# Performance work log

Measured on AMD Instinct MI355X. Metric: run time of the kernel, lower is better.

## Reference

```python
import jax, jax.numpy as jnp
import numpy as np

NVOC = 32000
DIM = 512
HID = 512
NLAYERS = 2
SEQ = 128
BATCH = 32


def setup_inputs() -> dict:
    key = jax.random.key(0)
    ks = jax.random.split(key, 8)
    tokens = jax.random.randint(ks[0], (SEQ, BATCH), 0, NVOC, dtype=jnp.int32)
    emb = jax.random.uniform(ks[1], (NVOC, DIM), minval=-0.1, maxval=0.1, dtype=jnp.float32)
    # xavier-uniform-ish init for gate matrices
    def xav(k, shape):
        fan_in, fan_out = shape[1], shape[0]
        lim = jnp.sqrt(6.0 / (fan_in + fan_out))
        return jax.random.uniform(k, shape, minval=-lim, maxval=lim, dtype=jnp.float32)
    W0 = xav(ks[2], (4 * HID, DIM))     # layer 0 input weights
    W1 = xav(ks[3], (4 * HID, HID))     # layer 1 input weights
    U0 = xav(ks[4], (4 * HID, HID))
    U1 = xav(ks[5], (4 * HID, HID))
    b = jnp.zeros((4 * HID,), jnp.float32)
    dec_w = jax.random.uniform(ks[6], (NVOC, HID), minval=-0.1, maxval=0.1, dtype=jnp.float32)
    dec_b = jnp.zeros((NVOC,), jnp.float32)
    return {"tokens": tokens, "emb": emb, "W0": W0, "W1": W1,
            "U0": U0, "U1": U1, "b": b, "dec_w": dec_w, "dec_b": dec_b}


def _lstm_forward(tokens, emb, W0, W1, U0, U1, b, dec_w, dec_b):
    # dropout in eval mode (identity)
    x = emb[tokens]  # [S, B, DIM]
    Ws = [W0, W1]
    Us = [U0, U1]
    h0 = jnp.zeros((NLAYERS, BATCH, HID), x.dtype)
    c0 = jnp.zeros((NLAYERS, BATCH, HID), x.dtype)

    def step(carry, x_t):
        h_tot, c_tot = carry
        new_h, new_c = [], []
        inp = x_t
        for l in range(NLAYERS):
            gates = inp @ Ws[l].T + h_tot[l] @ Us[l].T + b  # [B, 4H]
            i_g, f_g, g_g, o_g = jnp.split(gates, 4, axis=1)
            i_g = jax.nn.sigmoid(i_g)
            f_g = jax.nn.sigmoid(f_g)
            o_g = jax.nn.sigmoid(o_g)
            g_g = jnp.tanh(g_g)
            c_new = f_g * c_tot[l] + i_g * g_g
            h_new = o_g * jnp.tanh(c_new)
            new_h.append(h_new)
            new_c.append(c_new)
            inp = h_new
        return (jnp.stack(new_h), jnp.stack(new_c)), new_h[-1]

    (_, _), outs = jax.lax.scan(step, (h0, c0), x)  # outs: [S, B, HID]
    decoded = outs @ dec_w.T + dec_b  # [S, B, NVOC]
    return decoded


def reference(tokens, emb, W0, W1, U0, U1, b, dec_w, dec_b):
    return _lstm_forward(tokens, emb, W0, W1, U0, U1, b, dec_w, dec_b)
```

## Files before the change

### kernel.cpp

```cpp
#include <hip/hip_runtime.h>
#include <hip/hip_bf16.h>


#define NVOC 32000
#define DIM  512
#define HID  512
#define SEQ  128
#define BAT  32
#define NB   64
#define NDEC 192
#define NTILE (32 * 250)

typedef short s8v __attribute__((ext_vector_type(8)));
typedef short s4v __attribute__((ext_vector_type(4)));
typedef float f4v __attribute__((ext_vector_type(4)));
typedef unsigned long long u64;

__device__ __forceinline__ short f2bf(float f) {
    unsigned u = __builtin_bit_cast(unsigned, f);
    unsigned r = (u + 0x7fffu + ((u >> 16) & 1u)) >> 16;
    return (short)r;
}
__device__ __forceinline__ float bf2f(short s) {
    unsigned u = ((unsigned)(unsigned short)s) << 16;
    return __builtin_bit_cast(float, u);
}
__device__ __forceinline__ float sigm(float x) { return 1.f / (1.f + __expf(-x)); }
__device__ __forceinline__ float ftanh(float x) {
    float e = __expf(2.f * x);
    return 1.f - 2.f / (e + 1.f);
}

__device__ __forceinline__ f4v mf16(s8v a, s8v b, f4v c) {
    return __builtin_amdgcn_mfma_f32_16x16x32_bf16(a, b, c, 0, 0, 0);
}

__device__ __forceinline__ u64 cohload8(const short* p) {
    return __hip_atomic_load((const u64*)p, __ATOMIC_RELAXED,
                             __HIP_MEMORY_SCOPE_AGENT);
}
__device__ __forceinline__ void cohstore2(short* p, unsigned short v) {
    __hip_atomic_store((unsigned short*)p, v, __ATOMIC_RELAXED,
                       __HIP_MEMORY_SCOPE_AGENT);
}

__device__ __forceinline__ void pollwait(const unsigned* bar, int l,
                                         unsigned tA, unsigned tB) {
    const unsigned* fp = bar + l;
    const unsigned tgt = (l < 32) ? tA : tB;
    while (true) {
        unsigned v = __hip_atomic_load(fp, __ATOMIC_RELAXED,
                                       __HIP_MEMORY_SCOPE_AGENT);
        if (__all((int)(v >= tgt))) break;
    }
}
__device__ __forceinline__ void poll32s(const unsigned* f, int l, unsigned tgt) {
    const unsigned* p = f + (l & 31);
    while (true) {
        unsigned v = __hip_atomic_load(p, __ATOMIC_RELAXED,
                                       __HIP_MEMORY_SCOPE_AGENT);
        if (__all((int)(v >= tgt))) break;
        __builtin_amdgcn_s_sleep(16);
    }
}

__global__ __launch_bounds__(256) void prep_dec(const float* __restrict__ dw,
                                                short* __restrict__ dbf)
{
    int id = blockIdx.x * 256 + threadIdx.x;
    if (id >= (NVOC * DIM) / 4) return;
    int e = id * 4;
    float4 v = *(const float4*)(dw + e);
    s4v o; o[0] = f2bf(v.x); o[1] = f2bf(v.y); o[2] = f2bf(v.z); o[3] = f2bf(v.w);
    *(s4v*)(dbf + e) = o;
}

__global__ __launch_bounds__(256) void prep_w0(const float* __restrict__ W0,
                                               short* __restrict__ w0h,
                                               short* __restrict__ w0l)
{
    int id = blockIdx.x * 256 + threadIdx.x;
    if (id >= 2048 * 512) return;
    float v = W0[id];
    short h = f2bf(v);
    w0h[id] = h;
    w0l[id] = f2bf(v - bf2f(h));
}

__global__ __launch_bounds__(256) void embed_k(const int* __restrict__ toks,
                                               const float* __restrict__ emb,
                                               short* __restrict__ xemb)
{
    int id = blockIdx.x * 256 + threadIdx.x;
    if (id >= (SEQ * BAT * DIM) / 4) return;
    int e  = id * 4;
    int tb = e >> 9;
    int k4 = e & 511;
    int tok = toks[tb];
    float4 v = *(const float4*)(emb + (size_t)tok * DIM + k4);
    s4v o; o[0] = f2bf(v.x); o[1] = f2bf(v.y); o[2] = f2bf(v.z); o[3] = f2bf(v.w);
    *(s4v*)(xemb + e) = o;
}

__global__ __launch_bounds__(256) void init_k(short* __restrict__ hbuf,
                                              unsigned* __restrict__ bar)
{
    int id = blockIdx.x * 256 + threadIdx.x;
    if (id < 10 * BAT * HID) hbuf[id] = 0;
    if (id < 64) bar[id] = 0;
}

__global__ __launch_bounds__(256) void gx_gemm(
    const short* __restrict__ A,
    const short* __restrict__ Bh,
    const short* __restrict__ Bl,
    float* __restrict__ out)
{
    const int nb = blockIdx.x & 15, mb = blockIdx.x >> 4;
    const int m0 = mb * 128, n0 = nb * 128;
    __shared__ short Alds[128][40];
    __shared__ short Bhl[128][40];
    __shared__ short Bll[128][40];
    const int tid = threadIdx.x, l = tid & 63, w = tid >> 6;
    const int wr = w >> 1, wc = w & 1;
    const int lr = l & 15, kg = l >> 4;

    f4v acc[4][4];
    #pragma unroll
    for (int mi = 0; mi < 4; ++mi)
        #pragma unroll
        for (int ni = 0; ni < 4; ++ni) {
            acc[mi][ni][0] = 0.f; acc[mi][ni][1] = 0.f;
            acc[mi][ni][2] = 0.f; acc[mi][ni][3] = 0.f;
        }

    for (int kt = 0; kt < 16; ++kt) {
        #pragma unroll
        for (int i = 0; i < 2; ++i) {
            int c = tid + i * 256;
            int row = c >> 2, q = (c & 3) << 3;
            *(s8v*)&Alds[row][q] = *(const s8v*)(A  + (size_t)(m0 + row) * 512 + kt * 32 + q);
            *(s8v*)&Bhl[row][q]  = *(const s8v*)(Bh + (size_t)(n0 + row) * 512 + kt * 32 + q);
            *(s8v*)&Bll[row][q]  = *(const s8v*)(Bl + (size_t)(n0 + row) * 512 + kt * 32 + q);
        }
        __syncthreads();
        s8v af[4], bhf[4], blf[4];
        #pragma unroll
        for (int i = 0; i < 4; ++i) {
            af[i]  = *(const s8v*)&Alds[wr * 64 + i * 16 + lr][kg * 8];
            bhf[i] = *(const s8v*)&Bhl[wc * 64 + i * 16 + lr][kg * 8];
            blf[i] = *(const s8v*)&Bll[wc * 64 + i * 16 + lr][kg * 8];
        }
        #pragma unroll
        for (int mi = 0; mi < 4; ++mi)
            #pragma unroll
            for (int ni = 0; ni < 4; ++ni) {
                acc[mi][ni] = mf16(af[mi], bhf[ni], acc[mi][ni]);
                acc[mi][ni] = mf16(af[mi], blf[ni], acc[mi][ni]);
            }
        __syncthreads();
    }

    #pragma unroll
    for (int mi = 0; mi < 4; ++mi)
        #pragma unroll
        for (int ni = 0; ni < 4; ++ni) {
            int n = n0 + wc * 64 + ni * 16 + lr;
            #pragma unroll
            for (int r = 0; r < 4; ++r) {
                int m = m0 + wr * 64 + mi * 16 + kg * 4 + r;
                out[(size_t)m * 2048 + n] = acc[mi][ni][r];
            }
        }
}

__global__ __launch_bounds__(512, 1) void rnn_k(
    const float* __restrict__ W1f, const float* __restrict__ U0f,
    const float* __restrict__ U1f,
    const float* __restrict__ bias,
    const float* __restrict__ Gx,
    short* __restrict__ hbuf,
    short* __restrict__ adec,
    const short* __restrict__ dbf,
    const float* __restrict__ db,
    float* __restrict__ out,
    unsigned* __restrict__ bar)
{
    const int tid = threadIdx.x;
    const int bx  = blockIdx.x;
    const int w2  = tid >> 6;
    const int l   = tid & 63;
    const int lr  = l & 15;
    const int kg  = l >> 4;

    __shared__ short Alds[32][520];
    __shared__ float gbuf[2][4][16][33];
    __shared__ float pbuf[2][4][16][33];
    __shared__ s8v AdT[4][132];
    __shared__ s8v BdT[4][132];

    if (bx >= NB) {
        const int d  = bx - NB;
        const int wm = w2 >> 2;
        const int wn = w2 & 3;
        const int drow = tid >> 2, dq = tid & 3;
        int lastmb = -1;
        for (int tile = d; tile < NTILE; tile += NDEC) {
            const int mb = tile / 250, nbt = tile - mb * 250;
            const int m0 = mb * 128, n0 = nbt * 128;
            if (mb != lastmb) {
                if (w2 == 0) poll32s(bar + 32, l, (unsigned)(4 * mb + 5));
                __syncthreads();
                lastmb = mb;
            }
            f4v acc[4][2];
            #pragma unroll
            for (int mi = 0; mi < 4; ++mi)
                #pragma unroll
                for (int ni = 0; ni < 2; ++ni) {
                    acc[mi][ni][0] = 0.f; acc[mi][ni][1] = 0.f;
                    acc[mi][ni][2] = 0.f; acc[mi][ni][3] = 0.f;
                }
            for (int kt = 0; kt < 16; ++kt) {
                AdT[dq][drow] = *(const s8v*)(adec + (size_t)(m0 + drow) * 512 + kt * 32 + dq * 8);
                BdT[dq][drow] = *(const s8v*)(dbf  + (size_t)(n0 + drow) * 512 + kt * 32 + dq * 8);
                __syncthreads();
                s8v af[4], bfr[2];
                #pragma unroll
                for (int i = 0; i < 4; ++i)
                    af[i] = AdT[kg][wm * 64 + i * 16 + lr];
                #pragma unroll
                for (int j = 0; j < 2; ++j)
                    bfr[j] = BdT[kg][wn * 32 + j * 16 + lr];
                #pragma unroll
                for (int mi = 0; mi < 4; ++mi)
                    #pragma unroll
                    for (int ni = 0; ni < 2; ++ni)
                        acc[mi][ni] = mf16(af[mi], bfr[ni], acc[mi][ni]);
                __syncthreads();
            }
            #pragma unroll
            for (int mi = 0; mi < 4; ++mi)
                #pragma unroll
                for (int ni = 0; ni < 2; ++ni) {
                    int n = n0 + wn * 32 + ni * 16 + lr;
                    float bb = db[n];
                    #pragma unroll
                    for (int r = 0; r < 4; ++r) {
                        int m = m0 + wm * 64 + mi * 16 + kg * 4 + r;
                        out[(size_t)m * NVOC + n] = acc[mi][ni][r] + bb;
                    }
                }
        }
        return;
    }

    const int bl    = bx;
    const int layer = bl >> 5;
    const int j0    = (bl & 31) * 16;
    const int g     = w2 & 3;
    const int kh    = w2 >> 2;

    const int eb = tid >> 4;
    const int ej = tid & 15;
    const int jj = j0 + ej;
    const float bi = bias[jj];
    const float bf_ = bias[512 + jj];
    const float bg = bias[1024 + jj];
    const float bo = bias[1536 + jj];
    float cst = 0.f;

    short* h0r = hbuf;
    short* h1r = hbuf + 8 * BAT * HID;

    auto stageK512 = [&](const short* s) {
        u64 va[8];
        #pragma unroll
        for (int i = 0; i < 8; ++i) {
            int c = tid + i * 512;
            va[i] = cohload8(s + (c >> 7) * HID + (c & 127) * 4);
        }
        #pragma unroll
        for (int i = 0; i < 8; ++i) {
            int c = tid + i * 512;
            *(u64*)&Alds[c >> 7][(c & 127) * 4] = va[i];
        }
    };
    auto mfma8 = [&](const s8v* WH, const s8v* WL, float (&dst)[2][4][16][33]) {
        f4v a0h = {0.f, 0.f, 0.f, 0.f};
        f4v a0l = a0h, a1h = a0h, a1l = a0h;
        #pragma unroll
        for (int ks = 0; ks < 8; ++ks) {
            const int k = kh * 256 + ks * 32 + kg * 8;
            s8v a0 = *(const s8v*)&Alds[lr][k];
            s8v a1 = *(const s8v*)&Alds[16 + lr][k];
            a0h = mf16(a0, WH[ks], a0h);
            a0l = mf16(a0, WL[ks], a0l);
            a1h = mf16(a1, WH[ks], a1h);
            a1l = mf16(a1, WL[ks], a1l);
        }
        #pragma unroll
        for (int r = 0; r < 4; ++r) {
            dst[kh][g][lr][kg * 4 + r]      = a0h[r] + a0l[r];
            dst[kh][g][lr][16 + kg * 4 + r] = a1h[r] + a1l[r];
        }
    };
    const int gr = g * 512 + j0 + lr;
    auto loadw = [&](const float* M, s8v* WH, s8v* WL) {
        #pragma unroll
        for (int ks = 0; ks < 8; ++ks) {
            const float* src = M + (size_t)gr * 512 + kh * 256 + ks * 32 + kg * 8;
            float4 va = *(const float4*)src;
            float4 vb = *(const float4*)(src + 4);
            float vv[8] = {va.x, va.y, va.z, va.w, vb.x, vb.y, vb.z, vb.w};
            s8v hi, lo;
            #pragma unroll
            for (int e = 0; e < 8; ++e) {
                short h = f2bf(vv[e]);
                hi[e] = h; lo[e] = f2bf(vv[e] - bf2f(h));
            }
            WH[ks] = hi; WL[ks] = lo;
        }
    };

    if (layer == 0) {
        s8v wh[8], wl[8];
        loadw(U0f, wh, wl);
        for (int it = 0; it < SEQ; ++it) {
            const unsigned itu = (unsigned)it;
            const float* gp = Gx + ((size_t)it * BAT + eb) * 2048 + jj;
            float gx0 = gp[0], gx1 = gp[512], gx2 = gp[1024], gx3 = gp[1536];
            if (it > 0) {
                if (w2 == 0) pollwait(bar, l, itu, (it >= 7) ? itu - 6u : 0u);
                __syncthreads();
            }
            stageK512(h0r + ((it + 7) & 7) * (BAT * HID));
            __syncthreads();
            mfma8(wh, wl, gbuf);
            __syncthreads();
            float si = gbuf[0][0][ej][eb] + gbuf[1][0][ej][eb] + gx0;
            float sf = gbuf[0][1][ej][eb] + gbuf[1][1][ej][eb] + gx1;
            float sg = gbuf[0][2][ej][eb] + gbuf[1][2][ej][eb] + gx2;
            float so = gbuf[0][3][ej][eb] + gbuf[1][3][ej][eb] + gx3;
            float gi = sigm(si + bi);
            float gf = sigm(sf + bf_);
            float gg = ftanh(sg + bg);
            float go = sigm(so + bo);
            cst = gf * cst + gi * gg;
            unsigned short hs = (unsigned short)f2bf(go * ftanh(cst));
            cohstore2(h0r + (it & 7) * (BAT * HID) + eb * HID + jj, hs);
            asm volatile("s_waitcnt vmcnt(0)" ::: "memory");
            __syncthreads();
            if (tid == 0)
                __hip_atomic_store(bar + (bl & 31), itu + 1u,
                                   __ATOMIC_RELAXED, __HIP_MEMORY_SCOPE_AGENT);
        }
    } else {
        s8v whU[8], wlU[8], whW[8], wlW[8];
        loadw(U1f, whU, wlU);
        loadw(W1f, whW, wlW);
        if (w2 == 0) pollwait(bar, l, 1u, 0u);
        __syncthreads();
        stageK512(h0r);
        __syncthreads();
        mfma8(whW, wlW, pbuf);
        for (int it = 1; it <= SEQ; ++it) {
            const unsigned itu = (unsigned)it;
            if (w2 == 0) pollwait(bar, l, 0u, (it >= 2) ? itu : 0u);
            __syncthreads();
            stageK512(h1r + (it & 1) * (BAT * HID));
            __syncthreads();
            mfma8(whU, wlU, gbuf);
            __syncthreads();
            float si = gbuf[0][0][ej][eb] + gbuf[1][0][ej][eb]
                     + pbuf[0][0][ej][eb] + pbuf[1][0][ej][eb];
            float sf = gbuf[0][1][ej][eb] + gbuf[1][1][ej][eb]
                     + pbuf[0][1][ej][eb] + pbuf[1][1][ej][eb];
            float sg = gbuf[0][2][ej][eb] + gbuf[1][2][ej][eb]
                     + pbuf[0][2][ej][eb] + pbuf[1][2][ej][eb];
            float so = gbuf[0][3][ej][eb] + gbuf[1][3][ej][eb]
                     + pbuf[0][3][ej][eb] + pbuf[1][3][ej][eb];
            float gi = sigm(si + bi);
            float gf = sigm(sf + bf_);
            float gg = ftanh(sg + bg);
            float go = sigm(so + bo);
            cst = gf * cst + gi * gg;
            unsigned short hs = (unsigned short)f2bf(go * ftanh(cst));
            cohstore2(h1r + ((it + 1) & 1) * (BAT * HID) + eb * HID + jj, hs);
            cohstore2(adec + ((size_t)(it - 1) * BAT + eb) * HID + jj, hs);
            asm volatile("s_waitcnt vmcnt(0)" ::: "memory");
            __syncthreads();
            if (tid == 0)
                __hip_atomic_store(bar + 32 + (bl & 31), itu + 1u,
                                   __ATOMIC_RELAXED, __HIP_MEMORY_SCOPE_AGENT);
            if (it < SEQ) {
                if (w2 == 0) pollwait(bar, l, itu + 1u, 0u);
                __syncthreads();
                stageK512(h0r + (it & 7) * (BAT * HID));
                __syncthreads();
                mfma8(whW, wlW, pbuf);
            }
        }
    }
}

extern "C" void kernel_launch(void* const* d_in, const int* in_sizes, int n_in,
                              void* d_out, int out_size, void* d_ws, size_t ws_size,
                              hipStream_t stream)
{
    const int*   toks = (const int*)d_in[0];
    const float* emb  = (const float*)d_in[1];
    const float* W0   = (const float*)d_in[2];
    const float* W1   = (const float*)d_in[3];
    const float* U0   = (const float*)d_in[4];
    const float* U1   = (const float*)d_in[5];
    const float* bias = (const float*)d_in[6];
    const float* dw   = (const float*)d_in[7];
    const float* db   = (const float*)d_in[8];
    float* out = (float*)d_out;

    char* ws = (char*)d_ws;
    size_t off = 0;
    auto alloc = [&](size_t bytes) -> void* {
        void* p = ws + off;
        off += (bytes + 255) & ~(size_t)255;
        return p;
    };
    short*    dbf  = (short*)alloc((size_t)NVOC * DIM * 2);
    short*    xemb = (short*)alloc((size_t)SEQ * BAT * DIM * 2);
    short*    w0h  = (short*)alloc(2048ull * 512 * 2);
    short*    w0l  = (short*)alloc(2048ull * 512 * 2);
    float*    Gx   = (float*)alloc((size_t)SEQ * BAT * 2048 * 4);
    short*    hbuf = (short*)alloc(10ull * BAT * HID * 2);
    short*    adec = (short*)alloc((size_t)SEQ * BAT * HID * 2);
    unsigned* bar  = (unsigned*)alloc(256);

    prep_dec<<<(NVOC * DIM / 4 + 255) / 256, 256, 0, stream>>>(dw, dbf);
    prep_w0 <<<(2048 * 512 + 255) / 256, 256, 0, stream>>>(W0, w0h, w0l);
    embed_k <<<(SEQ * BAT * DIM / 4 + 255) / 256, 256, 0, stream>>>(toks, emb, xemb);
    init_k  <<<(10 * BAT * HID + 255) / 256, 256, 0, stream>>>(hbuf, bar);

    gx_gemm<<<32 * 16, 256, 0, stream>>>(xemb, w0h, w0l, Gx);

    rnn_k<<<NB + NDEC, 512, 0, stream>>>(W1, U0, U1, bias, Gx, hbuf, adec,
                                         dbf, db, out, bar);
}
```

Measured before the change: 793.4 us.

## Replace RNN flag barriers with sentinel-filled full-history h ring buffers

Each of the two recurrent layers now writes every timestep's hidden state into its own slot of a 129-slot buffer. Each buffer is pre-filled with an all-ones sentinel except slot 0. Consumers spin on the loaded 8-byte words until no 16-bit lane holds the sentinel, instead of polling per-block counters and doing a block barrier, waitcnt and flag store every step. This removes the per-step flag round-trip from the recurrence critical path. The layer-1 counter used by the decoder blocks is now only updated every 4 steps. In exchange, init writes a much larger buffer, and correctness relies on 0xFFFF never appearing as a real bf16 h value and on ordering of relaxed stores.

After: 699.0 us. 11.9% less time.

```diff
diff --git a/kernel.cpp b/kernel.cpp
--- a/kernel.cpp
+++ b/kernel.cpp
@@ -10,6 +10,7 @@
 #define NB   64
 #define NDEC 192
 #define NTILE (32 * 250)
+#define SLOT (BAT * HID)
 
 typedef short s8v __attribute__((ext_vector_type(8)));
 typedef short s4v __attribute__((ext_vector_type(4)));
@@ -44,16 +45,11 @@
                        __HIP_MEMORY_SCOPE_AGENT);
 }
 
-__device__ __forceinline__ void pollwait(const unsigned* bar, int l,
-                                         unsigned tA, unsigned tB) {
-    const unsigned* fp = bar + l;
-    const unsigned tgt = (l < 32) ? tA : tB;
-    while (true) {
-        unsigned v = __hip_atomic_load(fp, __ATOMIC_RELAXED,
-                                       __HIP_MEMORY_SCOPE_AGENT);
-        if (__all((int)(v >= tgt))) break;
-    }
-}
+__device__ __forceinline__ bool hasSent(u64 v) {
+    u64 n = ~v;
+    return ((n - 0x0001000100010001ull) & ~n & 0x8000800080008000ull) != 0ull;
+}
+
 __device__ __forceinline__ void poll32s(const unsigned* f, int l, unsigned tgt) {
     const unsigned* p = f + (l & 31);
     while (true) {
@@ -106,7 +102,12 @@
                                               unsigned* __restrict__ bar)
 {
     int id = blockIdx.x * 256 + threadIdx.x;
-    if (id < 10 * BAT * HID) hbuf[id] = 0;
+    const int ringU64 = 129 * SLOT / 4;
+    if (id < 2 * ringU64) {
+        int r = id % ringU64;
+        u64 v = (r < SLOT / 4) ? 0ull : 0xFFFFFFFFFFFFFFFFull;
+        ((u64*)hbuf)[id] = v;
+    }
     if (id < 64) bar[id] = 0;
 }
 
@@ -270,10 +271,10 @@
     const float bo = bias[1536 + jj];
     float cst = 0.f;
 
-    short* h0r = hbuf;
-    short* h1r = hbuf + 8 * BAT * HID;
-
-    auto stageK512 = [&](const short* s) {
+    short* ring0 = hbuf;
+    short* ring1 = hbuf + 129 * SLOT;
+
+    auto stageS = [&](const short* s) {
         u64 va[8];
         #pragma unroll
         for (int i = 0; i < 8; ++i) {
@@ -283,6 +284,8 @@
         #pragma unroll
         for (int i = 0; i < 8; ++i) {
             int c = tid + i * 512;
+            while (hasSent(va[i]))
+                va[i] = cohload8(s + (c >> 7) * HID + (c & 127) * 4);
             *(u64*)&Alds[c >> 7][(c & 127) * 4] = va[i];
         }
     };
@@ -327,14 +330,9 @@
         s8v wh[8], wl[8];
         loadw(U0f, wh, wl);
         for (int it = 0; it < SEQ; ++it) {
-            const unsigned itu = (unsigned)it;
             const float* gp = Gx + ((size_t)it * BAT + eb) * 2048 + jj;
             float gx0 = gp[0], gx1 = gp[512], gx2 = gp[1024], gx3 = gp[1536];
-            if (it > 0) {
-                if (w2 == 0) pollwait(bar, l, itu, (it >= 7) ? itu - 6u : 0u);
-                __syncthreads();
-            }
-            stageK512(h0r + ((it + 7) & 7) * (BAT * HID));
+            stageS(ring0 + (size_t)it * SLOT);
             __syncthreads();
             mfma8(wh, wl, gbuf);
             __syncthreads();
@@ -348,27 +346,17 @@
             float go = sigm(so + bo);
             cst = gf * cst + gi * gg;
             unsigned short hs = (unsigned short)f2bf(go * ftanh(cst));
-            cohstore2(h0r + (it & 7) * (BAT * HID) + eb * HID + jj, hs);
-            asm volatile("s_waitcnt vmcnt(0)" ::: "memory");
-            __syncthreads();
-            if (tid == 0)
-                __hip_atomic_store(bar + (bl & 31), itu + 1u,
-                                   __ATOMIC_RELAXED, __HIP_MEMORY_SCOPE_AGENT);
+            cohstore2(ring0 + (size_t)(it + 1) * SLOT + eb * HID + jj, hs);
         }
     } else {
         s8v whU[8], wlU[8], whW[8], wlW[8];
         loadw(U1f, whU, wlU);
         loadw(W1f, whW, wlW);
-        if (w2 == 0) pollwait(bar, l, 1u, 0u);
-        __syncthreads();
-        stageK512(h0r);
+        stageS(ring0 + 1 * SLOT);
         __syncthreads();
         mfma8(whW, wlW, pbuf);
         for (int it = 1; it <= SEQ; ++it) {
-            const unsigned itu = (unsigned)it;
-            if (w2 == 0) pollwait(bar, l, 0u, (it >= 2) ? itu : 0u);
-            __syncthreads();
-            stageK512(h1r + (it & 1) * (BAT * HID));
+            stageS(ring1 + (size_t)(it - 1) * SLOT);
             __syncthreads();
             mfma8(whU, wlU, gbuf);
             __syncthreads();
@@ -386,17 +374,17 @@
             float go = sigm(so + bo);
             cst = gf * cst + gi * gg;
             unsigned short hs = (unsigned short)f2bf(go * ftanh(cst));
-            cohstore2(h1r + ((it + 1) & 1) * (BAT * HID) + eb * HID + jj, hs);
+            cohstore2(ring1 + (size_t)it * SLOT + eb * HID + jj, hs);
             cohstore2(adec + ((size_t)(it - 1) * BAT + eb) * HID + jj, hs);
-            asm volatile("s_waitcnt vmcnt(0)" ::: "memory");
-            __syncthreads();
-            if (tid == 0)
-                __hip_atomic_store(bar + 32 + (bl & 31), itu + 1u,
-                                   __ATOMIC_RELAXED, __HIP_MEMORY_SCOPE_AGENT);
+            if ((it & 3) == 0 || it == SEQ) {
+                asm volatile("s_waitcnt vmcnt(0)" ::: "memory");
+                __syncthreads();
+                if (tid == 0)
+                    __hip_atomic_store(bar + 32 + (bl & 31), (unsigned)(it + 1),
+                                       __ATOMIC_RELAXED, __HIP_MEMORY_SCOPE_AGENT);
+            }
             if (it < SEQ) {
-                if (w2 == 0) pollwait(bar, l, itu + 1u, 0u);
-                __syncthreads();
-                stageK512(h0r + (it & 7) * (BAT * HID));
+                stageS(ring0 + (size_t)(it + 1) * SLOT);
                 __syncthreads();
                 mfma8(whW, wlW, pbuf);
             }
@@ -431,14 +419,17 @@
     short*    w0h  = (short*)alloc(2048ull * 512 * 2);
     short*    w0l  = (short*)alloc(2048ull * 512 * 2);
     float*    Gx   = (float*)alloc((size_t)SEQ * BAT * 2048 * 4);
-    short*    hbuf = (short*)alloc(10ull * BAT * HID * 2);
+    short*    hbuf = (short*)alloc(2ull * 129 * SLOT * 2);
     short*    adec = (short*)alloc((size_t)SEQ * BAT * HID * 2);
     unsigned* bar  = (unsigned*)alloc(256);
 
     prep_dec<<<(NVOC * DIM / 4 + 255) / 256, 256, 0, stream>>>(dw, dbf);
     prep_w0 <<<(2048 * 512 + 255) / 256, 256, 0, stream>>>(W0, w0h, w0l);
     embed_k <<<(SEQ * BAT * DIM / 4 + 255) / 256, 256, 0, stream>>>(toks, emb, xemb);
-    init_k  <<<(10 * BAT * HID + 255) / 256, 256, 0, stream>>>(hbuf, bar);
+    {
+        int ringU64 = 2 * 129 * SLOT / 4;
+        init_k<<<(ringU64 + 255) / 256, 256, 0, stream>>>(hbuf, bar);
+    }
 
     gx_gemm<<<32 * 16, 256, 0, stream>>>(xemb, w0h, w0l, Gx);
 
```
